# Performance work log

Hardware: AMD Instinct MI355X
Metric: run time of the kernel (lower is better)

The kernel has to match this reference:

```python
import jax, jax.numpy as jnp
import numpy as np

VOCAB = 101
EMB = 32
HID = 32


def setup_inputs() -> dict:
    key = jax.random.key(0)
    k = jax.random.split(key, 7)
    B, T = 4096, 512
    x = jax.random.randint(k[0], (B, T), 0, VOCAB, dtype=jnp.int32)
    emb = jax.random.normal(k[1], (VOCAB, EMB), dtype=jnp.float32) * 0.1
    # gate order: i, f, g, o (concatenated along last dim)
    Wx = jax.random.normal(k[2], (EMB, 4 * HID), dtype=jnp.float32) * 0.1
    Wh = jax.random.normal(k[3], (HID, 4 * HID), dtype=jnp.float32) * 0.1
    b = jax.random.normal(k[4], (4 * HID,), dtype=jnp.float32) * 0.1
    W_fc = jax.random.normal(k[5], (HID, 2), dtype=jnp.float32) * 0.1
    b_fc = jax.random.normal(k[6], (2,), dtype=jnp.float32) * 0.1
    return {"x": x, "emb": emb, "Wx": Wx, "Wh": Wh, "b": b, "W_fc": W_fc, "b_fc": b_fc}


def _lstm_last_h(xe, Wx, Wh, b):
    # xe: [B, T, EMB]
    B = xe.shape[0]
    # precompute input contributions for all timesteps: [T, B, 4H]
    xg = jnp.einsum('bte,eh->tbh', xe, Wx) + b
    h0 = jnp.zeros((B, HID), xe.dtype)
    c0 = jnp.zeros((B, HID), xe.dtype)

    def step(carry, xt):
        h, c = carry
        g = xt + h @ Wh  # [B, 4H]
        i, f, gg, o = jnp.split(g, 4, axis=-1)
        c = jax.nn.sigmoid(f) * c + jax.nn.sigmoid(i) * jnp.tanh(gg)
        h = jax.nn.sigmoid(o) * jnp.tanh(c)
        return (h, c), None

    (h, c), _ = jax.lax.scan(step, (h0, c0), xg)
    return h  # last hidden state == hidden_seq[:, -1, :]


def reference(x, emb, Wx, Wh, b, W_fc, b_fc):
    xe = emb[x]  # [B, T, EMB]
    h = _lstm_last_h(xe, Wx, Wh, b)
    return h @ W_fc + b_fc  # [B, 2]
```

## Files before the change

### kernel.cpp

```cpp
#include <hip/hip_runtime.h>
#include <stdint.h>

#define T_LEN 512
#define VOCAB 101
#define GP    132
#define XPB   516
#define HPW   20

typedef short short8 __attribute__((ext_vector_type(8)));
typedef float f32x4  __attribute__((ext_vector_type(4)));

#define LOG2E 1.442695041f
#define L2E2  2.885390082f

__device__ __forceinline__ float asF(uint32_t u) {
    union { uint32_t i; float f; } x; x.i = u; return x.f;
}
__device__ __forceinline__ float bf2f(uint16_t u) { return asF(((uint32_t)u) << 16); }
__device__ __forceinline__ float bf_lo(uint32_t u) { return asF(u << 16); }
__device__ __forceinline__ float bf_hi(uint32_t u) { return asF(u & 0xFFFF0000u); }
__device__ __forceinline__ uint16_t f2bf(float f) {
    union { float f; uint32_t i; } x; x.f = f;
    return (uint16_t)((x.i + 0x7FFFu + ((x.i >> 16) & 1u)) >> 16);
}
__device__ __forceinline__ float getw(const void* p, int i, bool isbf) {
    return isbf ? bf2f(((const uint16_t*)p)[i]) : ((const float*)p)[i];
}
__device__ __forceinline__ bool detect_bf16(const void* embp) {
    const uint16_t* u = (const uint16_t*)embp;
    int sane = 0;
    for (int i = 0; i < 64; ++i) {
        uint16_t v = u[i];
        int e = (v >> 7) & 0xFF;
        sane += ((e >= 100 && e <= 140) || ((v & 0x7FFFu) == 0)) ? 1 : 0;
    }
    return sane >= 56;
}

#define GATES(S, CST, HOUT)                                                     \
  {                                                                             \
    float ai = __builtin_amdgcn_exp2f(-(S)[0]);                                 \
    float af = __builtin_amdgcn_exp2f(-(S)[1]);                                 \
    float ag = __builtin_amdgcn_exp2f(-(S)[2]);                                 \
    float ao = __builtin_amdgcn_exp2f(-(S)[3]);                                 \
    float uu = 1.f + ai, ww = 1.f + ag, zz = 1.f + af;                          \
    float uw = uu * ww;                                                         \
    float num = __builtin_fmaf(__builtin_fmaf(ww, -L2E2, 2.f * L2E2), zz,       \
                               (CST) * uw);                                     \
    float cs = num * __builtin_amdgcn_rcpf(zz * uw);                            \
    (CST) = cs;                                                                 \
    float ac = __builtin_amdgcn_exp2f(-cs);                                     \
    float t1 = 1.f + ac;                                                        \
    (HOUT) = (2.f - t1) * __builtin_amdgcn_rcpf((1.f + ao) * t1);               \
  }

__global__ __launch_bounds__(256, 1) void lstm_fused(
    const int* __restrict__ x, const void* __restrict__ emb,
    const void* __restrict__ Wx, const void* __restrict__ Wh,
    const void* __restrict__ bias, const void* __restrict__ Wfc,
    const void* __restrict__ bfc, void* __restrict__ out)
{
    __shared__ __align__(16) float    Gl[VOCAB * GP];
    __shared__ __align__(16) uint8_t  xt8[16 * XPB];
    __shared__ __align__(16) uint32_t hbuf[2 * 16 * HPW];

    const int tid = threadIdx.x;
    const int wl  = tid & 63;
    const int w   = tid >> 6;
    const int n   = wl & 15;
    const int q   = wl >> 4;
    const int b0  = blockIdx.x * 16;

    const bool isbf = detect_bf16(emb);

    for (int idx = tid; idx < VOCAB * 128; idx += 256) {
        int v = idx >> 7, cc = idx & 127;
        int u = cc >> 2, g = cc & 3;
        int col = 32 * g + u;
        float acc = getw(bias, col, isbf);
        #pragma unroll 8
        for (int k = 0; k < 32; ++k)
            acc += getw(emb, v * 32 + k, isbf) * getw(Wx, k * 128 + col, isbf);
        Gl[v * GP + cc] = acc * ((g == 2) ? L2E2 : LOG2E);
    }
    for (int i = tid; i < 2048; i += 256) {
        int row = i >> 7, c4 = i & 127;
        int4 vv = *(const int4*)&x[(b0 + row) * T_LEN + (c4 << 2)];
        uint32_t p = (uint32_t)(vv.x & 255) | ((uint32_t)(vv.y & 255) << 8) |
                     ((uint32_t)(vv.z & 255) << 16) | ((uint32_t)(vv.w & 255) << 24);
        ((uint32_t*)&xt8[row * XPB])[c4] = p;
    }
    for (int i = tid; i < 2 * 16 * HPW; i += 256) hbuf[i] = 0;

    short8 afr0, afr1;
    {
        const int gte = n & 3, ul = n >> 2;
        const float sc = (gte == 2) ? L2E2 : LOG2E;
        const int base = 32 * gte + 8 * w + 2 * ul;
        union { short8 v; uint16_t s[8]; } u0, u1;
        #pragma unroll
        for (int jj = 0; jj < 8; ++jj) {
            int kk = 8 * q + jj;
            u0.s[jj] = f2bf(getw(Wh, kk * 128 + base,     isbf) * sc);
            u1.s[jj] = f2bf(getw(Wh, kk * 128 + base + 1, isbf) * sc);
        }
        afr0 = u0.v; afr1 = u1.v;
    }
    __syncthreads();

    const int u0i = 8 * w + 2 * q;
    float c0 = 0.f, c1 = 0.f;
    const uint8_t* xr = &xt8[n * XPB];

    f32x4 gc0, gc1;
    {
        const f32x4* gp = (const f32x4*)&Gl[(int)xr[0] * GP + u0i * 4];
        gc0 = gp[0]; gc1 = gp[1];
    }
    int tokA = xr[1];

    for (int t = 0; t < T_LEN; ++t) {
        const uint32_t* hr = &hbuf[(t & 1) * (16 * HPW)];
        uint32_t*       hw = &hbuf[((t & 1) ^ 1) * (16 * HPW)];
        short8 bfrag = *(const short8*)&hr[n * HPW + 4 * q];
        f32x4 s0 = __builtin_amdgcn_mfma_f32_16x16x32_bf16(afr0, bfrag, gc0, 0, 0, 0);
        f32x4 s1 = __builtin_amdgcn_mfma_f32_16x16x32_bf16(afr1, bfrag, gc1, 0, 0, 0);
        f32x4 gn0, gn1;
        {
            const f32x4* gp = (const f32x4*)&Gl[tokA * GP + u0i * 4];
            gn0 = gp[0]; gn1 = gp[1];
        }
        int tokN = xr[(t + 2) & (T_LEN - 1)];
        float h0, h1;
        GATES(s0, c0, h0);
        GATES(s1, c1, h1);
        uint32_t hp;
        asm("v_cvt_pk_bf16_f32 %0, %1, %2" : "=v"(hp) : "v"(h0), "v"(h1));
        hw[n * HPW + 4 * w + q] = hp;
        gc0 = gn0; gc1 = gn1; tokA = tokN;
        __syncthreads();
    }

    if (tid < 32) {
        int row = tid >> 1, cc = tid & 1;
        float acc = getw(bfc, cc, isbf);
        #pragma unroll 8
        for (int k = 0; k < 32; ++k) {
            uint32_t d = hbuf[row * HPW + (k >> 1)];
            float hval = (k & 1) ? bf_hi(d) : bf_lo(d);
            acc += hval * getw(Wfc, k * 2 + cc, isbf);
        }
        int oidx = (b0 + row) * 2 + cc;
        if (isbf) ((uint16_t*)out)[oidx] = f2bf(acc);
        else      ((float*)out)[oidx]    = acc;
    }
}

extern "C" void kernel_launch(void* const* d_in, const int* in_sizes, int n_in,
                              void* d_out, int out_size, void* d_ws, size_t ws_size,
                              hipStream_t stream) {
    (void)in_sizes; (void)n_in; (void)d_ws; (void)ws_size; (void)out_size;
    const int* x = (const int*)d_in[0];
    lstm_fused<<<dim3(256), dim3(256), 0, stream>>>(
        x, d_in[1], d_in[2], d_in[3], d_in[4], d_in[5], d_in[6], d_out);
}
```

Baseline: 283.8 us.

## Store gate table as bf16 and software-pipeline LSTM step with manual waitcnts

The precomputed token-to-gate table is now stored in LDS as bf16 instead of fp32, halving the per-step gather to a single 16-byte read. The time loop is unrolled by two, prefetches gate rows and tokens two steps ahead, and uses sched_barrier plus explicit lgkmcnt waits and a raw s_barrier in place of __syncthreads. The goal is to shorten the serial per-step critical path by overlapping LDS latency with MFMA and gate math. In exchange the input contribution loses precision in bf16, and the hand-placed waitcnt values must exactly match the compiler's LDS issue order to stay correct.

```diff
diff --git a/kernel.cpp b/kernel.cpp
--- a/kernel.cpp
+++ b/kernel.cpp
@@ -3,9 +3,10 @@
 
 #define T_LEN 512
 #define VOCAB 101
-#define GP    132
+#define GSP   136
 #define XPB   516
 #define HPW   20
+#define HB1   (16 * HPW)
 
 typedef short short8 __attribute__((ext_vector_type(8)));
 typedef float f32x4  __attribute__((ext_vector_type(4)));
@@ -54,13 +55,46 @@
     (HOUT) = (2.f - t1) * __builtin_amdgcn_rcpf((1.f + ao) * t1);               \
   }
 
+#define STEP_T(HRoff, HWoff, TOFF, TKUSE, TKDEF)                                    \
+  {                                                                                 \
+    const uint32_t* hr = &hbuf[HRoff];                                              \
+    uint32_t*       hw = &hbuf[HWoff];                                              \
+    short8 bfrag = *(const short8*)&hr[n * HPW + 4 * q];                            \
+    short8 graw  = *(const short8*)&Gl2[adr1 + (u0i << 2)];                         \
+    TKDEF = xr[TOFF];                                                               \
+    __builtin_amdgcn_sched_barrier(0);                                              \
+    f32x4 gc0, gc1;                                                                 \
+    { union { short8 v; uint32_t d[4]; } ug; ug.v = grawP;                          \
+      gc0[0] = bf_lo(ug.d[0]); gc0[1] = bf_hi(ug.d[0]);                             \
+      gc0[2] = bf_lo(ug.d[1]); gc0[3] = bf_hi(ug.d[1]);                             \
+      gc1[0] = bf_lo(ug.d[2]); gc1[1] = bf_hi(ug.d[2]);                             \
+      gc1[2] = bf_lo(ug.d[3]); gc1[3] = bf_hi(ug.d[3]); }                           \
+    adr1 = (TKUSE) * GSP;                                                           \
+    __builtin_amdgcn_sched_barrier(0);                                              \
+    asm volatile("s_waitcnt lgkmcnt(2)" ::: "memory");                              \
+    __builtin_amdgcn_sched_barrier(0);                                              \
+    f32x4 s0 = __builtin_amdgcn_mfma_f32_16x16x32_bf16(afr0, bfrag, gc0, 0, 0, 0);  \
+    f32x4 s1 = __builtin_amdgcn_mfma_f32_16x16x32_bf16(afr1, bfrag, gc1, 0, 0, 0);  \
+    float h0, h1;                                                                   \
+    GATES(s0, c0, h0);                                                              \
+    GATES(s1, c1, h1);                                                              \
+    uint32_t hp;                                                                    \
+    asm("v_cvt_pk_bf16_f32 %0, %1, %2" : "=v"(hp) : "v"(h0), "v"(h1));              \
+    hw[n * HPW + 4 * w + q] = hp;                                                   \
+    grawP = graw;                                                                   \
+    __builtin_amdgcn_sched_barrier(0);                                              \
+    asm volatile("s_waitcnt lgkmcnt(0)" ::: "memory");                              \
+    __builtin_amdgcn_s_barrier();                                                   \
+    __builtin_amdgcn_sched_barrier(0);                                              \
+  }
+
 __global__ __launch_bounds__(256, 1) void lstm_fused(
     const int* __restrict__ x, const void* __restrict__ emb,
     const void* __restrict__ Wx, const void* __restrict__ Wh,
     const void* __restrict__ bias, const void* __restrict__ Wfc,
     const void* __restrict__ bfc, void* __restrict__ out)
 {
-    __shared__ __align__(16) float    Gl[VOCAB * GP];
+    __shared__ __align__(16) uint16_t Gl2[VOCAB * GSP];
     __shared__ __align__(16) uint8_t  xt8[16 * XPB];
     __shared__ __align__(16) uint32_t hbuf[2 * 16 * HPW];
 
@@ -81,7 +115,7 @@
         #pragma unroll 8
         for (int k = 0; k < 32; ++k)
             acc += getw(emb, v * 32 + k, isbf) * getw(Wx, k * 128 + col, isbf);
-        Gl[v * GP + cc] = acc * ((g == 2) ? L2E2 : LOG2E);
+        Gl2[v * GSP + cc] = f2bf(acc * ((g == 2) ? L2E2 : LOG2E));
     }
     for (int i = tid; i < 2048; i += 256) {
         int row = i >> 7, c4 = i & 127;
@@ -89,6 +123,10 @@
         uint32_t p = (uint32_t)(vv.x & 255) | ((uint32_t)(vv.y & 255) << 8) |
                      ((uint32_t)(vv.z & 255) << 16) | ((uint32_t)(vv.w & 255) << 24);
         ((uint32_t*)&xt8[row * XPB])[c4] = p;
+    }
+    for (int i = tid; i < 48; i += 256) {
+        int row = i / 3, j = i % 3;
+        xt8[row * XPB + 512 + j] = (uint8_t)x[(b0 + row) * T_LEN + j];
     }
     for (int i = tid; i < 2 * 16 * HPW; i += 256) hbuf[i] = 0;
 
@@ -112,34 +150,21 @@
     float c0 = 0.f, c1 = 0.f;
     const uint8_t* xr = &xt8[n * XPB];
 
-    f32x4 gc0, gc1;
+    short8 grawP;
+    int adr1, tkA, tkB;
     {
-        const f32x4* gp = (const f32x4*)&Gl[(int)xr[0] * GP + u0i * 4];
-        gc0 = gp[0]; gc1 = gp[1];
+        int t0 = xr[0], t1 = xr[1];
+        tkA = xr[2];
+        grawP = *(const short8*)&Gl2[t0 * GSP + (u0i << 2)];
+        adr1  = t1 * GSP;
     }
-    int tokA = xr[1];
 
-    for (int t = 0; t < T_LEN; ++t) {
-        const uint32_t* hr = &hbuf[(t & 1) * (16 * HPW)];
-        uint32_t*       hw = &hbuf[((t & 1) ^ 1) * (16 * HPW)];
-        short8 bfrag = *(const short8*)&hr[n * HPW + 4 * q];
-        f32x4 s0 = __builtin_amdgcn_mfma_f32_16x16x32_bf16(afr0, bfrag, gc0, 0, 0, 0);
-        f32x4 s1 = __builtin_amdgcn_mfma_f32_16x16x32_bf16(afr1, bfrag, gc1, 0, 0, 0);
-        f32x4 gn0, gn1;
-        {
-            const f32x4* gp = (const f32x4*)&Gl[tokA * GP + u0i * 4];
-            gn0 = gp[0]; gn1 = gp[1];
-        }
-        int tokN = xr[(t + 2) & (T_LEN - 1)];
-        float h0, h1;
-        GATES(s0, c0, h0);
-        GATES(s1, c1, h1);
-        uint32_t hp;
-        asm("v_cvt_pk_bf16_f32 %0, %1, %2" : "=v"(hp) : "v"(h0), "v"(h1));
-        hw[n * HPW + 4 * w + q] = hp;
-        gc0 = gn0; gc1 = gn1; tokA = tokN;
-        __syncthreads();
+    for (int t = 0; t < T_LEN; t += 2) {
+        STEP_T(0,   HB1, t + 3, tkA, tkB);
+        STEP_T(HB1, 0,   t + 4, tkB, tkA);
     }
+
+    __syncthreads();
 
     if (tid < 32) {
         int row = tid >> 1, cc = tid & 1;
```

New measurement: 288.0 us. No clear change (+1.5%).

## Keep LSTM recurrence wave-local via ds_bpermute, removing per-step block barriers

Applied to the files above, without the earlier changes.

Each wavefront now owns two batch rows and computes all 128 gate columns with eight MFMAs per step. The hidden state is redistributed in registers with shuffles and ds_bpermute instead of going through shared memory with a __syncthreads each timestep. The gate lookup table is stored as bf16 to cut LDS use, and blocks cover 8 rows with 512 blocks and two blocks per CU. The trade is four times the MFMA work per row, plus lane-selection overhead and lower precision on the input-gate contributions.

```diff
diff --git a/kernel.cpp b/kernel.cpp
--- a/kernel.cpp
+++ b/kernel.cpp
@@ -3,9 +3,8 @@
 
 #define T_LEN 512
 #define VOCAB 101
-#define GP    132
+#define GSP   140
 #define XPB   516
-#define HPW   20
 
 typedef short short8 __attribute__((ext_vector_type(8)));
 typedef float f32x4  __attribute__((ext_vector_type(4)));
@@ -37,12 +36,12 @@
     return sane >= 56;
 }
 
-#define GATES(S, CST, HOUT)                                                     \
+#define GATES4(PI, PF, PG, PO, CST, HOUT)                                       \
   {                                                                             \
-    float ai = __builtin_amdgcn_exp2f(-(S)[0]);                                 \
-    float af = __builtin_amdgcn_exp2f(-(S)[1]);                                 \
-    float ag = __builtin_amdgcn_exp2f(-(S)[2]);                                 \
-    float ao = __builtin_amdgcn_exp2f(-(S)[3]);                                 \
+    float ai = __builtin_amdgcn_exp2f(-(PI));                                   \
+    float af = __builtin_amdgcn_exp2f(-(PF));                                   \
+    float ag = __builtin_amdgcn_exp2f(-(PG));                                   \
+    float ao = __builtin_amdgcn_exp2f(-(PO));                                   \
     float uu = 1.f + ai, ww = 1.f + ag, zz = 1.f + af;                          \
     float uw = uu * ww;                                                         \
     float num = __builtin_fmaf(__builtin_fmaf(ww, -L2E2, 2.f * L2E2), zz,       \
@@ -54,105 +53,133 @@
     (HOUT) = (2.f - t1) * __builtin_amdgcn_rcpf((1.f + ao) * t1);               \
   }
 
-__global__ __launch_bounds__(256, 1) void lstm_fused(
+__global__ __launch_bounds__(256, 2) void lstm_fused(
     const int* __restrict__ x, const void* __restrict__ emb,
     const void* __restrict__ Wx, const void* __restrict__ Wh,
     const void* __restrict__ bias, const void* __restrict__ Wfc,
     const void* __restrict__ bfc, void* __restrict__ out)
 {
-    __shared__ __align__(16) float    Gl[VOCAB * GP];
-    __shared__ __align__(16) uint8_t  xt8[16 * XPB];
-    __shared__ __align__(16) uint32_t hbuf[2 * 16 * HPW];
+    __shared__ __align__(16) uint16_t Gl2[VOCAB * GSP];
+    __shared__ __align__(16) uint8_t  xt8[8 * XPB];
 
     const int tid = threadIdx.x;
     const int wl  = tid & 63;
-    const int w   = tid >> 6;
+    const int lw  = tid >> 6;
     const int n   = wl & 15;
     const int q   = wl >> 4;
-    const int b0  = blockIdx.x * 16;
+    const int b0  = blockIdx.x * 8;
+    const int u   = n + 16 * (q >> 1);
+    const int rowG = 2 * lw + (q & 1);
 
     const bool isbf = detect_bf16(emb);
 
     for (int idx = tid; idx < VOCAB * 128; idx += 256) {
         int v = idx >> 7, cc = idx & 127;
-        int u = cc >> 2, g = cc & 3;
-        int col = 32 * g + u;
+        int uu = cc >> 2, g = cc & 3;
+        int col = 32 * g + uu;
         float acc = getw(bias, col, isbf);
         #pragma unroll 8
         for (int k = 0; k < 32; ++k)
             acc += getw(emb, v * 32 + k, isbf) * getw(Wx, k * 128 + col, isbf);
-        Gl[v * GP + cc] = acc * ((g == 2) ? L2E2 : LOG2E);
+        Gl2[v * GSP + cc] = f2bf(acc * ((g == 2) ? L2E2 : LOG2E));
     }
-    for (int i = tid; i < 2048; i += 256) {
+    for (int i = tid; i < 1024; i += 256) {
         int row = i >> 7, c4 = i & 127;
         int4 vv = *(const int4*)&x[(b0 + row) * T_LEN + (c4 << 2)];
         uint32_t p = (uint32_t)(vv.x & 255) | ((uint32_t)(vv.y & 255) << 8) |
                      ((uint32_t)(vv.z & 255) << 16) | ((uint32_t)(vv.w & 255) << 24);
         ((uint32_t*)&xt8[row * XPB])[c4] = p;
     }
-    for (int i = tid; i < 2 * 16 * HPW; i += 256) hbuf[i] = 0;
+    if (tid < 16) {
+        int row = tid >> 1, j = tid & 1;
+        xt8[row * XPB + 512 + j] = (uint8_t)x[(b0 + row) * T_LEN + j];
+    }
 
-    short8 afr0, afr1;
-    {
-        const int gte = n & 3, ul = n >> 2;
-        const float sc = (gte == 2) ? L2E2 : LOG2E;
-        const int base = 32 * gte + 8 * w + 2 * ul;
-        union { short8 v; uint16_t s[8]; } u0, u1;
+    short8 bfr[8];
+    #pragma unroll
+    for (int jt = 0; jt < 8; ++jt) {
+        const float sc = ((jt >> 1) == 2) ? L2E2 : LOG2E;
+        union { short8 v; uint16_t s[8]; } ub;
         #pragma unroll
-        for (int jj = 0; jj < 8; ++jj) {
-            int kk = 8 * q + jj;
-            u0.s[jj] = f2bf(getw(Wh, kk * 128 + base,     isbf) * sc);
-            u1.s[jj] = f2bf(getw(Wh, kk * 128 + base + 1, isbf) * sc);
-        }
-        afr0 = u0.v; afr1 = u1.v;
+        for (int jj = 0; jj < 8; ++jj)
+            ub.s[jj] = f2bf(getw(Wh, (8 * q + jj) * 128 + 16 * jt + n, isbf) * sc);
+        bfr[jt] = ub.v;
     }
     __syncthreads();
 
-    const int u0i = 8 * w + 2 * q;
-    float c0 = 0.f, c1 = 0.f;
-    const uint8_t* xr = &xt8[n * XPB];
+    const uint8_t* xr = &xt8[rowG * XPB];
 
-    f32x4 gc0, gc1;
-    {
-        const f32x4* gp = (const f32x4*)&Gl[(int)xr[0] * GP + u0i * 4];
-        gc0 = gp[0]; gc1 = gp[1];
-    }
+    #define MKADR(J2) (4 * (32 * ((4 * q + (J2)) >> 3) + 16 * (n & 1) + \
+                            2 * ((4 * q + (J2)) & 7)))
+    const int adr0 = MKADR(0), adr1 = MKADR(1), adr2 = MKADR(2), adr3 = MKADR(3);
+    const bool selR = (q & 1) != 0;
+    const bool selH = ((q >> 1) & 1) != 0;
+    const bool par  = (n & 1) != 0;
+
+    float c0 = 0.f, hlast = 0.f;
+    int aw0 = 0, aw1 = 0, aw2 = 0, aw3 = 0;
+    uint64_t grC = *(const uint64_t*)&Gl2[(int)xr[0] * GSP + 4 * u];
     int tokA = xr[1];
+    const f32x4 Z = {0.f, 0.f, 0.f, 0.f};
 
     for (int t = 0; t < T_LEN; ++t) {
-        const uint32_t* hr = &hbuf[(t & 1) * (16 * HPW)];
-        uint32_t*       hw = &hbuf[((t & 1) ^ 1) * (16 * HPW)];
-        short8 bfrag = *(const short8*)&hr[n * HPW + 4 * q];
-        f32x4 s0 = __builtin_amdgcn_mfma_f32_16x16x32_bf16(afr0, bfrag, gc0, 0, 0, 0);
-        f32x4 s1 = __builtin_amdgcn_mfma_f32_16x16x32_bf16(afr1, bfrag, gc1, 0, 0, 0);
-        f32x4 gn0, gn1;
-        {
-            const f32x4* gp = (const f32x4*)&Gl[tokA * GP + u0i * 4];
-            gn0 = gp[0]; gn1 = gp[1];
-        }
-        int tokN = xr[(t + 2) & (T_LEN - 1)];
-        float h0, h1;
-        GATES(s0, c0, h0);
-        GATES(s1, c1, h1);
-        uint32_t hp;
-        asm("v_cvt_pk_bf16_f32 %0, %1, %2" : "=v"(hp) : "v"(h0), "v"(h1));
-        hw[n * HPW + 4 * w + q] = hp;
-        gc0 = gn0; gc1 = gn1; tokA = tokN;
-        __syncthreads();
+        union { int d[4]; short8 v; } ua;
+        ua.d[0] = aw0; ua.d[1] = aw1; ua.d[2] = aw2; ua.d[3] = aw3;
+        short8 af = ua.v;
+        f32x4 s0 = __builtin_amdgcn_mfma_f32_16x16x32_bf16(af, bfr[0], Z, 0, 0, 0);
+        f32x4 s1 = __builtin_amdgcn_mfma_f32_16x16x32_bf16(af, bfr[1], Z, 0, 0, 0);
+        f32x4 s2 = __builtin_amdgcn_mfma_f32_16x16x32_bf16(af, bfr[2], Z, 0, 0, 0);
+        f32x4 s3 = __builtin_amdgcn_mfma_f32_16x16x32_bf16(af, bfr[3], Z, 0, 0, 0);
+        f32x4 s4 = __builtin_amdgcn_mfma_f32_16x16x32_bf16(af, bfr[4], Z, 0, 0, 0);
+        f32x4 s5 = __builtin_amdgcn_mfma_f32_16x16x32_bf16(af, bfr[5], Z, 0, 0, 0);
+        f32x4 s6 = __builtin_amdgcn_mfma_f32_16x16x32_bf16(af, bfr[6], Z, 0, 0, 0);
+        f32x4 s7 = __builtin_amdgcn_mfma_f32_16x16x32_bf16(af, bfr[7], Z, 0, 0, 0);
+        uint64_t grN = *(const uint64_t*)&Gl2[tokA * GSP + 4 * u];
+        tokA = xr[t + 2];
+        float a0 = selR ? s0[1] : s0[0], b0v = selR ? s1[1] : s1[0];
+        float pi = selH ? b0v : a0;
+        float a1 = selR ? s2[1] : s2[0], b1v = selR ? s3[1] : s3[0];
+        float pf = selH ? b1v : a1;
+        float a2 = selR ? s4[1] : s4[0], b2v = selR ? s5[1] : s5[0];
+        float pg = selH ? b2v : a2;
+        float a3 = selR ? s6[1] : s6[0], b3v = selR ? s7[1] : s7[0];
+        float po = selH ? b3v : a3;
+        uint32_t glo = (uint32_t)grC, ghi = (uint32_t)(grC >> 32);
+        pi += bf_lo(glo); pf += bf_hi(glo);
+        pg += bf_lo(ghi); po += bf_hi(ghi);
+        float h0;
+        GATES4(pi, pf, pg, po, c0, h0);
+        hlast = h0;
+        float ho  = __shfl_xor(h0, 1);
+        float plo = par ? ho : h0;
+        float phi = par ? h0 : ho;
+        uint32_t hd;
+        asm("v_cvt_pk_bf16_f32 %0, %1, %2" : "=v"(hd) : "v"(plo), "v"(phi));
+        aw0 = __builtin_amdgcn_ds_bpermute(adr0, (int)hd);
+        aw1 = __builtin_amdgcn_ds_bpermute(adr1, (int)hd);
+        aw2 = __builtin_amdgcn_ds_bpermute(adr2, (int)hd);
+        aw3 = __builtin_amdgcn_ds_bpermute(adr3, (int)hd);
+        grC = grN;
     }
 
-    if (tid < 32) {
-        int row = tid >> 1, cc = tid & 1;
-        float acc = getw(bfc, cc, isbf);
-        #pragma unroll 8
-        for (int k = 0; k < 32; ++k) {
-            uint32_t d = hbuf[row * HPW + (k >> 1)];
-            float hval = (k & 1) ? bf_hi(d) : bf_lo(d);
-            acc += hval * getw(Wfc, k * 2 + cc, isbf);
+    float p0 = hlast * getw(Wfc, u * 2 + 0, isbf);
+    float p1 = hlast * getw(Wfc, u * 2 + 1, isbf);
+    p0 += __shfl_xor(p0, 1);  p1 += __shfl_xor(p1, 1);
+    p0 += __shfl_xor(p0, 2);  p1 += __shfl_xor(p1, 2);
+    p0 += __shfl_xor(p0, 4);  p1 += __shfl_xor(p1, 4);
+    p0 += __shfl_xor(p0, 8);  p1 += __shfl_xor(p1, 8);
+    p0 += __shfl_xor(p0, 32); p1 += __shfl_xor(p1, 32);
+    if (wl == 0 || wl == 16) {
+        int grow = b0 + rowG;
+        float o0 = p0 + getw(bfc, 0, isbf);
+        float o1 = p1 + getw(bfc, 1, isbf);
+        if (isbf) {
+            ((uint16_t*)out)[grow * 2 + 0] = f2bf(o0);
+            ((uint16_t*)out)[grow * 2 + 1] = f2bf(o1);
+        } else {
+            ((float*)out)[grow * 2 + 0] = o0;
+            ((float*)out)[grow * 2 + 1] = o1;
         }
-        int oidx = (b0 + row) * 2 + cc;
-        if (isbf) ((uint16_t*)out)[oidx] = f2bf(acc);
-        else      ((float*)out)[oidx]    = acc;
     }
 }
 
@@ -161,6 +188,6 @@
                               hipStream_t stream) {
     (void)in_sizes; (void)n_in; (void)d_ws; (void)ws_size; (void)out_size;
     const int* x = (const int*)d_in[0];
-    lstm_fused<<<dim3(256), dim3(256), 0, stream>>>(
+    lstm_fused<<<dim3(512), dim3(256), 0, stream>>>(
         x, d_in[1], d_in[2], d_in[3], d_in[4], d_in[5], d_in[6], d_out);
 }
```

Measured after the change: 381.0 us. +34.2%, slower.
